# Performance work log

Hardware: AMD Instinct MI355X
Metric: run time of the kernel (lower is better)

Reference implementation:

```python
import jax, jax.numpy as jnp
import numpy as np

B, T, D, H = 4, 2048, 1024, 16
HD = D // H


def setup_inputs() -> dict:
    key = jax.random.key(0)
    k1, k2, k3 = jax.random.split(key, 3)
    x = jax.random.normal(k1, (B, T, D), dtype=jnp.float32)
    # xavier-uniform-like scale for the projections
    s_qkv = float(np.sqrt(6.0 / (D + 3 * D)))
    s_o = float(np.sqrt(6.0 / (D + D)))
    W_qkv = jax.random.uniform(k2, (D, 3 * D), minval=-s_qkv, maxval=s_qkv, dtype=jnp.float32)
    W_o = jax.random.uniform(k3, (D, D), minval=-s_o, maxval=s_o, dtype=jnp.float32)
    b_qkv = jnp.zeros((3 * D,), dtype=jnp.float32)
    b_o = jnp.zeros((D,), dtype=jnp.float32)
    # pad out the last 256 key positions to exercise the padding-mask path
    key_padding_mask = jnp.zeros((B, T), dtype=bool).at[:, -256:].set(True)
    return {"x": x, "W_qkv": W_qkv, "b_qkv": b_qkv, "W_o": W_o, "b_o": b_o,
            "key_padding_mask": key_padding_mask}


def reference(x, W_qkv, b_qkv, W_o, b_o, key_padding_mask):
    Bx, Tx, Dx = x.shape
    # fused QKV projection
    qkv = x @ W_qkv + b_qkv                      # [B,T,3D]
    q, k, v = jnp.split(qkv, 3, axis=-1)
    to_heads = lambda t: t.reshape(Bx, Tx, H, HD).transpose(0, 2, 1, 3)  # [B,H,T,Hd]
    q, k, v = to_heads(q), to_heads(k), to_heads(v)
    scale = 1.0 / np.sqrt(HD).astype(np.float32)
    scores = jnp.einsum('bhqd,bhkd->bhqk', q, k) * scale   # [B,H,T,T]
    causal = jnp.triu(jnp.ones((Tx, Tx), dtype=bool), k=1)  # True above diagonal => masked
    mask = key_padding_mask[:, None, None, :] | causal[None, None, :, :]
    scores = jnp.where(mask, -jnp.inf, scores)
    A = jax.nn.softmax(scores, axis=-1)
    ctx = jnp.einsum('bhqk,bhkd->bhqd', A, v)               # [B,H,T,Hd]
    y = ctx.transpose(0, 2, 1, 3).reshape(Bx, Tx, Dx)
    return y @ W_o + b_o
```

## Files before the change

kernel.cpp:

```cpp
#include <hip/hip_runtime.h>
#include <cstdint>
#include <cstddef>

typedef __bf16 bf16x8 __attribute__((ext_vector_type(8)));
typedef float f32x4 __attribute__((ext_vector_type(4)));
typedef float f32x16 __attribute__((ext_vector_type(16)));
typedef unsigned short u16x4 __attribute__((ext_vector_type(4)));
typedef unsigned int u32x4 __attribute__((ext_vector_type(4)));

__device__ __forceinline__ unsigned short f2bf(float f) {
  union { float f; unsigned u; } v; v.f = f;
  unsigned r = (v.u + 0x7FFF + ((v.u >> 16) & 1)) >> 16;
  return (unsigned short)r;
}

__device__ __forceinline__ unsigned pkbf(float x, float y) {
  unsigned short a = __builtin_bit_cast(unsigned short, (__bf16)x);
  unsigned short b = __builtin_bit_cast(unsigned short, (__bf16)y);
  return (unsigned)a | ((unsigned)b << 16);
}

__device__ __forceinline__ void gl2lds16(const void* g, void* l) {
  __builtin_amdgcn_global_load_lds(
      (const __attribute__((address_space(1))) void*)g,
      (__attribute__((address_space(3))) void*)l,
      16, 0, 0);
}

__global__ __launch_bounds__(256) void cast_f32_bf16(
    const float* __restrict__ in, unsigned short* __restrict__ out, int n) {
  int i = (blockIdx.x * 256 + threadIdx.x) * 4;
  if (i >= n) return;
  float4 v = *(const float4*)(in + i);
  u16x4 o;
  o[0] = f2bf(v.x); o[1] = f2bf(v.y); o[2] = f2bf(v.z); o[3] = f2bf(v.w);
  *(u16x4*)(out + i) = o;
}

__global__ __launch_bounds__(256) void transpose_cast(
    const float* __restrict__ in, unsigned short* __restrict__ out, int R, int C) {
  __shared__ float t[32][33];
  int c0 = blockIdx.x * 32, r0 = blockIdx.y * 32;
  int tx = threadIdx.x, ty = threadIdx.y;
#pragma unroll
  for (int j = 0; j < 4; ++j)
    t[ty + j * 8][tx] = in[(size_t)(r0 + ty + j * 8) * C + c0 + tx];
  __syncthreads();
#pragma unroll
  for (int j = 0; j < 4; ++j)
    out[(size_t)(c0 + ty + j * 8) * R + r0 + tx] = f2bf(t[tx][ty + j * 8]);
}

__global__ __launch_bounds__(256) void prep_pad(
    const int* __restrict__ mask, float* __restrict__ padd, int* __restrict__ kmax, int n) {
  int i = blockIdx.x * 256 + threadIdx.x;
  if (i >= n) return;
  int mv = mask[i];
  padd[i] = mv ? -1e30f : 0.0f;
  int key = mv ? 0 : ((i & 2047) + 1);
#pragma unroll
  for (int off = 32; off; off >>= 1) key = max(key, __shfl_xor(key, off, 64));
  if ((threadIdx.x & 63) == 0) atomicMax(&kmax[i >> 11], key);
}

template <int EPI>
__global__ __launch_bounds__(256) void gemm_bt(
    const unsigned short* __restrict__ A, const unsigned short* __restrict__ Bm,
    const float* __restrict__ bias, float* __restrict__ outF,
    unsigned short* __restrict__ Qb, unsigned short* __restrict__ Kb,
    unsigned short* __restrict__ Vt, int M, int N, int K) {
  __shared__ unsigned short As[2 * 128 * 32];
  __shared__ unsigned short Bs[2 * 128 * 32];
  const int tid = threadIdx.x;
  const int bm = blockIdx.x * 128;
  const int bn = blockIdx.y * 128;
  const int wave = tid >> 6, lane = tid & 63;
  const int wm = (wave >> 1) * 64, wn = (wave & 1) * 64;
  const int lr = lane & 15, lq = lane >> 4;

  f32x4 acc[4][4] = {};

  const int c0 = tid, c1 = tid + 256;
  const int rA0 = c0 >> 2, colA0 = (c0 & 3) * 8;
  const int rA1 = c1 >> 2, colA1 = (c1 & 3) * 8;

  auto stage = [&](int buf, int k0) {
    gl2lds16(A + (size_t)(bm + rA0) * K + k0 + colA0, As + buf * 4096 + c0 * 8);
    gl2lds16(A + (size_t)(bm + rA1) * K + k0 + colA1, As + buf * 4096 + c1 * 8);
    gl2lds16(Bm + (size_t)(bn + rA0) * K + k0 + colA0, Bs + buf * 4096 + c0 * 8);
    gl2lds16(Bm + (size_t)(bn + rA1) * K + k0 + colA1, Bs + buf * 4096 + c1 * 8);
  };

  stage(0, 0);
  int cur = 0;
  for (int k0 = 0; k0 < K; k0 += 32) {
    __syncthreads();
    if (k0 + 32 < K) stage(cur ^ 1, k0 + 32);
    const unsigned short* Asb = As + cur * 4096;
    const unsigned short* Bsb = Bs + cur * 4096;
    bf16x8 af[4], bfr[4];
#pragma unroll
    for (int mi = 0; mi < 4; ++mi)
      af[mi] = *(const bf16x8*)(Asb + (wm + mi * 16 + lr) * 32 + lq * 8);
#pragma unroll
    for (int nj = 0; nj < 4; ++nj)
      bfr[nj] = *(const bf16x8*)(Bsb + (wn + nj * 16 + lr) * 32 + lq * 8);
#pragma unroll
    for (int mi = 0; mi < 4; ++mi)
#pragma unroll
      for (int nj = 0; nj < 4; ++nj)
        acc[mi][nj] = __builtin_amdgcn_mfma_f32_16x16x32_bf16(af[mi], bfr[nj], acc[mi][nj], 0, 0, 0);
    cur ^= 1;
  }

#pragma unroll
  for (int mi = 0; mi < 4; ++mi) {
#pragma unroll
    for (int nj = 0; nj < 4; ++nj) {
#pragma unroll
      for (int r = 0; r < 4; ++r) {
        int m = bm + wm + mi * 16 + lq * 4 + r;
        int n = bn + wn + nj * 16 + lr;
        float v = acc[mi][nj][r] + bias[n];
        if (EPI == 0) {
          int b = m >> 11, t = m & 2047;
          int part = n >> 10, d = n & 1023;
          int h = d >> 6, hd = d & 63;
          size_t qk = ((size_t)(b * 16 + h) * 2048 + t) * 64 + hd;
          if (part == 0)      Qb[qk] = f2bf(v * 0.18033688011112042f);
          else if (part == 1) Kb[qk] = f2bf(v);
          else                Vt[((size_t)(b * 16 + h) * 64 + hd) * 2048 + t] = f2bf(v);
        } else {
          outF[(size_t)m * N + n] = v;
        }
      }
    }
  }
}

__global__ __launch_bounds__(256, 4) void flash_attn(
    const unsigned short* __restrict__ Qb, const unsigned short* __restrict__ Kb,
    const unsigned short* __restrict__ Vt, const int* __restrict__ kmax,
    unsigned short* __restrict__ ctx) {
  __shared__ unsigned short lds[16384];

  const int bid = blockIdx.x;
  const int halfg = bid >> 9;
  const int rb = bid & 511;
  const int bh = rb & 63;
  const int j0 = rb >> 6;
  const int j = halfg ? (15 - j0) : j0;
  const int blockQ = j << 7;
  const int b = bh >> 4, h = bh & 15;
  const int tid = threadIdx.x;
  const int wave = tid >> 6, lane = tid & 63;
  const int l31 = lane & 31, hi = lane >> 5;
  const int qw = blockQ + wave * 32;

  const unsigned short* Qh = Qb + (size_t)bh * 2048 * 64;
  const unsigned short* Kh = Kb + (size_t)bh * 2048 * 64;
  const unsigned short* Vh = Vt + (size_t)bh * 64 * 2048;
  unsigned short* ctxBase = ctx + (size_t)b * 2048 * 1024 + h * 64;

  const int kmaxRaw = kmax[b];
  const int kcapC = (kmaxRaw + 63) >> 6;
  const int lastB = min((blockQ + 127) >> 6, kcapC - 1);
  const int diagI = qw >> 6;

  bf16x8 qf[4];
#pragma unroll
  for (int ds = 0; ds < 4; ++ds)
    qf[ds] = *(const bf16x8*)(Qh + (size_t)(qw + l31) * 64 + ds * 16 + hi * 8);

  f32x16 O[2] = {};
  float mR = -1e30f, lR = 0.f;

  const int trow = tid >> 3, tslot = tid & 7;

  auto stage = [&](int bufI, int kcS) {
#pragma unroll
    for (int rnd = 0; rnd < 2; ++rnd) {
      int row = rnd * 32 + trow;
      int sl = tslot ^ (row & 7);
      gl2lds16(Kh + (size_t)(kcS + row) * 64 + sl * 8,
               lds + bufI * 8192 + rnd * 2048 + tid * 8);
      gl2lds16(Vh + (size_t)row * 2048 + kcS + sl * 8,
               lds + bufI * 8192 + 4096 + rnd * 2048 + tid * 8);
    }
  };

  stage(0, 0);
  int cur = 0;
  for (int i = 0; i <= lastB; ++i) {
    __syncthreads();
    if (i < lastB) stage(cur ^ 1, (i + 1) << 6);
    if (i <= diagI) {
      const int kc = i << 6;
      const unsigned short* Ksb = lds + cur * 8192;
      const unsigned short* Vsb = Ksb + 4096;

      f32x16 S[2] = {};
      __builtin_amdgcn_s_setprio(1);
#pragma unroll
      for (int kt = 0; kt < 2; ++kt) {
        const int row = kt * 32 + l31;
        const int rx = row & 7;
#pragma unroll
        for (int ds = 0; ds < 4; ++ds) {
          bf16x8 kfr = *(const bf16x8*)(Ksb + row * 64 + (((ds * 2 + hi) ^ rx) << 3));
          S[kt] = __builtin_amdgcn_mfma_f32_32x32x16_bf16(kfr, qf[ds], S[kt], 0, 0, 0);
        }
      }
      __builtin_amdgcn_s_setprio(0);

      const bool isDiag = (i == diagI);
      if (isDiag || (kc + 64 > kmaxRaw)) {
        const int q = qw + l31;
#pragma unroll
        for (int kt = 0; kt < 2; ++kt)
#pragma unroll
          for (int rr = 0; rr < 16; ++rr) {
            int key = kc + kt * 32 + (rr & 3) + ((rr >> 2) << 3) + (hi << 2);
            if ((isDiag && key > q) || key >= kmaxRaw) S[kt][rr] = -1e30f;
          }
      }

      {
        float v[16];
#pragma unroll
        for (int rr = 0; rr < 16; ++rr) v[rr] = fmaxf(S[0][rr], S[1][rr]);
#pragma unroll
        for (int st = 8; st; st >>= 1)
#pragma unroll
          for (int rr = 0; rr < st; ++rr) v[rr] = fmaxf(v[rr], v[rr + st]);
        float mx = fmaxf(v[0], __shfl_xor(v[0], 32, 64));
        float mnew = fmaxf(mR, mx);
        float a = __builtin_amdgcn_exp2f(mR - mnew);
        mR = mnew;
#pragma unroll
        for (int kt = 0; kt < 2; ++kt)
#pragma unroll
          for (int rr = 0; rr < 16; ++rr)
            S[kt][rr] = __builtin_amdgcn_exp2f(S[kt][rr] - mnew);
        float sacc[16];
#pragma unroll
        for (int rr = 0; rr < 16; ++rr) sacc[rr] = S[0][rr] + S[1][rr];
#pragma unroll
        for (int st = 8; st; st >>= 1)
#pragma unroll
          for (int rr = 0; rr < st; ++rr) sacc[rr] += sacc[rr + st];
        float sum = sacc[0] + __shfl_xor(sacc[0], 32, 64);
        lR = lR * a + sum;
#pragma unroll
        for (int mt = 0; mt < 2; ++mt)
#pragma unroll
          for (int rr = 0; rr < 16; ++rr) O[mt][rr] *= a;
      }
      bf16x8 pf[2][2];
#pragma unroll
      for (int kt = 0; kt < 2; ++kt) {
        unsigned a0 = pkbf(S[kt][0], S[kt][1]);
        unsigned a1 = pkbf(S[kt][2], S[kt][3]);
        unsigned b0 = pkbf(S[kt][4], S[kt][5]);
        unsigned b1 = pkbf(S[kt][6], S[kt][7]);
        unsigned c0 = pkbf(S[kt][8], S[kt][9]);
        unsigned c1 = pkbf(S[kt][10], S[kt][11]);
        unsigned d0 = pkbf(S[kt][12], S[kt][13]);
        unsigned d1 = pkbf(S[kt][14], S[kt][15]);
        unsigned s0 = __shfl_xor(hi ? a0 : b0, 32, 64);
        unsigned s1 = __shfl_xor(hi ? a1 : b1, 32, 64);
        unsigned s2 = __shfl_xor(hi ? c0 : d0, 32, 64);
        unsigned s3 = __shfl_xor(hi ? c1 : d1, 32, 64);
        u32x4 f0, f1;
        f0[0] = hi ? s0 : a0; f0[1] = hi ? s1 : a1;
        f0[2] = hi ? b0 : s0; f0[3] = hi ? b1 : s1;
        f1[0] = hi ? s2 : c0; f1[1] = hi ? s3 : c1;
        f1[2] = hi ? d0 : s2; f1[3] = hi ? d1 : s3;
        pf[kt][0] = __builtin_bit_cast(bf16x8, f0);
        pf[kt][1] = __builtin_bit_cast(bf16x8, f1);
      }

      __builtin_amdgcn_s_setprio(1);
      const int vx = l31 & 7;
#pragma unroll
      for (int kt = 0; kt < 2; ++kt)
#pragma unroll
        for (int ks = 0; ks < 2; ++ks) {
          const int slot = kt * 4 + ks * 2 + hi;
          bf16x8 v0 = *(const bf16x8*)(Vsb + l31 * 64 + ((slot ^ vx) << 3));
          bf16x8 v1 = *(const bf16x8*)(Vsb + (32 + l31) * 64 + ((slot ^ vx) << 3));
          O[0] = __builtin_amdgcn_mfma_f32_32x32x16_bf16(v0, pf[kt][ks], O[0], 0, 0, 0);
          O[1] = __builtin_amdgcn_mfma_f32_32x32x16_bf16(v1, pf[kt][ks], O[1], 0, 0, 0);
        }
      __builtin_amdgcn_s_setprio(0);
    }
    cur ^= 1;
  }

  {
    float linv = 1.0f / lR;
    const int q = qw + l31;
    unsigned short* cp = ctxBase + (size_t)q * 1024;
#pragma unroll
    for (int mt = 0; mt < 2; ++mt)
#pragma unroll
      for (int g = 0; g < 4; ++g) {
        u16x4 o4;
#pragma unroll
        for (int rr = 0; rr < 4; ++rr) o4[rr] = f2bf(O[mt][4 * g + rr] * linv);
        *(u16x4*)(cp + mt * 32 + 8 * g + 4 * hi) = o4;
      }
  }
}

extern "C" void kernel_launch(void* const* d_in, const int* in_sizes, int n_in,
                              void* d_out, int out_size, void* d_ws, size_t ws_size,
                              hipStream_t stream) {
  const float* x    = (const float*)d_in[0];
  const float* Wqkv = (const float*)d_in[1];
  const float* bqkv = (const float*)d_in[2];
  const float* Wo   = (const float*)d_in[3];
  const float* bo   = (const float*)d_in[4];
  const int*   mask = (const int*)d_in[5];
  float* out = (float*)d_out;

  unsigned short* ws = (unsigned short*)d_ws;
  const size_t SZ_X = (size_t)8192 * 1024;
  unsigned short* xb    = ws;
  unsigned short* WqkvT = xb + SZ_X;
  unsigned short* WoT   = WqkvT + (size_t)3072 * 1024;
  unsigned short* Qb    = WoT + (size_t)1024 * 1024;
  unsigned short* Kb    = Qb + SZ_X;
  unsigned short* Vt    = Kb + SZ_X;
  float*          padd  = (float*)(Vt + SZ_X);
  int*            kmax  = (int*)(padd + 8192);
  unsigned short* ctx   = xb;

  hipMemsetAsync(kmax, 0, 4 * sizeof(int), stream);
  cast_f32_bf16<<<8192, 256, 0, stream>>>(x, xb, (int)SZ_X);
  transpose_cast<<<dim3(96, 32), dim3(32, 8), 0, stream>>>(Wqkv, WqkvT, 1024, 3072);
  transpose_cast<<<dim3(32, 32), dim3(32, 8), 0, stream>>>(Wo, WoT, 1024, 1024);
  prep_pad<<<32, 256, 0, stream>>>(mask, padd, kmax, 8192);
  gemm_bt<0><<<dim3(64, 24), 256, 0, stream>>>(xb, WqkvT, bqkv, nullptr, Qb, Kb, Vt,
                                               8192, 3072, 1024);
  flash_attn<<<1024, 256, 0, stream>>>(Qb, Kb, Vt, kmax, ctx);
  gemm_bt<1><<<dim3(64, 8), 256, 0, stream>>>(ctx, WoT, bo, out, nullptr, nullptr, nullptr,
                                              8192, 1024, 1024);
}
```

Baseline: 273.7 us.

## Fuse preprocessing kernels and rework GEMM with triple-buffered swizzled LDS tiles

Merges the x cast, the two weight transpose-casts and the padding scan into one launch, and drops the unused padd buffer. The GEMM moves to 512-thread blocks with 256x128 tiles, a K-step of 64, and three LDS stages in dynamic shared memory. LDS rows use an XOR swizzle to avoid bank conflicts, and explicit vmcnt waits plus s_setprio around the MFMA burst help overlap loads with compute. This cuts launch overhead and raises GEMM data reuse and latency hiding, at the cost of large LDS use (144KB) that limits occupancy and fewer blocks for the output projection GEMM.

After: 261.6 us. 4.4% less time.

```diff
diff --git a/kernel.cpp b/kernel.cpp
--- a/kernel.cpp
+++ b/kernel.cpp
@@ -27,90 +27,128 @@
       16, 0, 0);
 }
 
-__global__ __launch_bounds__(256) void cast_f32_bf16(
-    const float* __restrict__ in, unsigned short* __restrict__ out, int n) {
-  int i = (blockIdx.x * 256 + threadIdx.x) * 4;
-  if (i >= n) return;
-  float4 v = *(const float4*)(in + i);
-  u16x4 o;
-  o[0] = f2bf(v.x); o[1] = f2bf(v.y); o[2] = f2bf(v.z); o[3] = f2bf(v.w);
-  *(u16x4*)(out + i) = o;
-}
-
-__global__ __launch_bounds__(256) void transpose_cast(
-    const float* __restrict__ in, unsigned short* __restrict__ out, int R, int C) {
+__global__ __launch_bounds__(256) void prep_fused(
+    const float* __restrict__ x, unsigned short* __restrict__ xb,
+    const float* __restrict__ Wqkv, unsigned short* __restrict__ WqkvT,
+    const float* __restrict__ Wo, unsigned short* __restrict__ WoT,
+    const int* __restrict__ mask, int* __restrict__ kmax) {
   __shared__ float t[32][33];
-  int c0 = blockIdx.x * 32, r0 = blockIdx.y * 32;
-  int tx = threadIdx.x, ty = threadIdx.y;
-#pragma unroll
-  for (int j = 0; j < 4; ++j)
-    t[ty + j * 8][tx] = in[(size_t)(r0 + ty + j * 8) * C + c0 + tx];
-  __syncthreads();
-#pragma unroll
-  for (int j = 0; j < 4; ++j)
-    out[(size_t)(c0 + ty + j * 8) * R + r0 + tx] = f2bf(t[tx][ty + j * 8]);
-}
-
-__global__ __launch_bounds__(256) void prep_pad(
-    const int* __restrict__ mask, float* __restrict__ padd, int* __restrict__ kmax, int n) {
-  int i = blockIdx.x * 256 + threadIdx.x;
-  if (i >= n) return;
-  int mv = mask[i];
-  padd[i] = mv ? -1e30f : 0.0f;
-  int key = mv ? 0 : ((i & 2047) + 1);
-#pragma unroll
-  for (int off = 32; off; off >>= 1) key = max(key, __shfl_xor(key, off, 64));
-  if ((threadIdx.x & 63) == 0) atomicMax(&kmax[i >> 11], key);
+  const int bid = blockIdx.x, tid = threadIdx.x;
+  if (bid < 4096) {
+    size_t i = ((size_t)bid * 256 + tid) * 4;
+#pragma unroll
+    for (int c = 0; c < 2; ++c) {
+      float4 v = *(const float4*)(x + i);
+      u16x4 o;
+      o[0] = f2bf(v.x); o[1] = f2bf(v.y); o[2] = f2bf(v.z); o[3] = f2bf(v.w);
+      *(u16x4*)(xb + i) = o;
+      i += (size_t)4096 * 256 * 4;
+    }
+  } else if (bid < 4096 + 3072) {
+    const int b2 = bid - 4096;
+    const int c0 = (b2 % 96) * 32, r0 = (b2 / 96) * 32;
+    const int tx = tid & 31, ty = tid >> 5;
+#pragma unroll
+    for (int j = 0; j < 4; ++j)
+      t[ty + j * 8][tx] = Wqkv[(size_t)(r0 + ty + j * 8) * 3072 + c0 + tx];
+    __syncthreads();
+#pragma unroll
+    for (int j = 0; j < 4; ++j)
+      WqkvT[(size_t)(c0 + ty + j * 8) * 1024 + r0 + tx] = f2bf(t[tx][ty + j * 8]);
+  } else if (bid < 8192) {
+    const int b3 = bid - (4096 + 3072);
+    const int c0 = (b3 & 31) * 32, r0 = (b3 >> 5) * 32;
+    const int tx = tid & 31, ty = tid >> 5;
+#pragma unroll
+    for (int j = 0; j < 4; ++j)
+      t[ty + j * 8][tx] = Wo[(size_t)(r0 + ty + j * 8) * 1024 + c0 + tx];
+    __syncthreads();
+#pragma unroll
+    for (int j = 0; j < 4; ++j)
+      WoT[(size_t)(c0 + ty + j * 8) * 1024 + r0 + tx] = f2bf(t[tx][ty + j * 8]);
+  } else {
+    const int i = (bid - 8192) * 256 + tid;
+    int mv = mask[i];
+    int key = mv ? 0 : ((i & 2047) + 1);
+#pragma unroll
+    for (int off = 32; off; off >>= 1) key = max(key, __shfl_xor(key, off, 64));
+    if ((tid & 63) == 0) atomicMax(&kmax[i >> 11], key);
+  }
 }
 
 template <int EPI>
-__global__ __launch_bounds__(256) void gemm_bt(
+__global__ __launch_bounds__(512, 2) void gemm_bt(
     const unsigned short* __restrict__ A, const unsigned short* __restrict__ Bm,
     const float* __restrict__ bias, float* __restrict__ outF,
     unsigned short* __restrict__ Qb, unsigned short* __restrict__ Kb,
     unsigned short* __restrict__ Vt, int M, int N, int K) {
-  __shared__ unsigned short As[2 * 128 * 32];
-  __shared__ unsigned short Bs[2 * 128 * 32];
+  extern __shared__ unsigned short lds[];
   const int tid = threadIdx.x;
-  const int bm = blockIdx.x * 128;
+  const int bm = blockIdx.x * 256;
   const int bn = blockIdx.y * 128;
   const int wave = tid >> 6, lane = tid & 63;
-  const int wm = (wave >> 1) * 64, wn = (wave & 1) * 64;
+  const int wm4 = wave >> 1, wn2 = wave & 1;
   const int lr = lane & 15, lq = lane >> 4;
+  const int NT = K >> 6;
 
   f32x4 acc[4][4] = {};
 
-  const int c0 = tid, c1 = tid + 256;
-  const int rA0 = c0 >> 2, colA0 = (c0 & 3) * 8;
-  const int rA1 = c1 >> 2, colA1 = (c1 & 3) * 8;
+  const int tr = tid >> 3, ts = tid & 7;
+  const int srcsl = (ts ^ (tr & 7)) << 3;
 
   auto stage = [&](int buf, int k0) {
-    gl2lds16(A + (size_t)(bm + rA0) * K + k0 + colA0, As + buf * 4096 + c0 * 8);
-    gl2lds16(A + (size_t)(bm + rA1) * K + k0 + colA1, As + buf * 4096 + c1 * 8);
-    gl2lds16(Bm + (size_t)(bn + rA0) * K + k0 + colA0, Bs + buf * 4096 + c0 * 8);
-    gl2lds16(Bm + (size_t)(bn + rA1) * K + k0 + colA1, Bs + buf * 4096 + c1 * 8);
+#pragma unroll
+    for (int r = 0; r < 4; ++r) {
+      int row = r * 64 + tr;
+      gl2lds16(A + (size_t)(bm + row) * K + k0 + srcsl,
+               lds + buf * 24576 + r * 4096 + tid * 8);
+    }
+#pragma unroll
+    for (int r = 0; r < 2; ++r) {
+      int row = r * 64 + tr;
+      gl2lds16(Bm + (size_t)(bn + row) * K + k0 + srcsl,
+               lds + buf * 24576 + 16384 + r * 4096 + tid * 8);
+    }
   };
 
   stage(0, 0);
-  int cur = 0;
-  for (int k0 = 0; k0 < K; k0 += 32) {
-    __syncthreads();
-    if (k0 + 32 < K) stage(cur ^ 1, k0 + 32);
-    const unsigned short* Asb = As + cur * 4096;
-    const unsigned short* Bsb = Bs + cur * 4096;
-    bf16x8 af[4], bfr[4];
-#pragma unroll
-    for (int mi = 0; mi < 4; ++mi)
-      af[mi] = *(const bf16x8*)(Asb + (wm + mi * 16 + lr) * 32 + lq * 8);
-#pragma unroll
-    for (int nj = 0; nj < 4; ++nj)
-      bfr[nj] = *(const bf16x8*)(Bsb + (wn + nj * 16 + lr) * 32 + lq * 8);
-#pragma unroll
-    for (int mi = 0; mi < 4; ++mi)
-#pragma unroll
-      for (int nj = 0; nj < 4; ++nj)
-        acc[mi][nj] = __builtin_amdgcn_mfma_f32_16x16x32_bf16(af[mi], bfr[nj], acc[mi][nj], 0, 0, 0);
-    cur ^= 1;
+  stage(1, 64);
+  int bT = 0, bT2 = 2;
+  const int rx = lr & 7;
+  for (int T = 0; T < NT; ++T) {
+    if (T < NT - 1) {
+      asm volatile("s_waitcnt vmcnt(6)" ::: "memory");
+    } else {
+      asm volatile("s_waitcnt vmcnt(0)" ::: "memory");
+    }
+    __builtin_amdgcn_s_barrier();
+    __builtin_amdgcn_sched_barrier(0);
+    if (T + 2 < NT) stage(bT2, (T + 2) << 6);
+    const unsigned short* Ab = lds + bT * 24576;
+    const unsigned short* Bb = Ab + 16384;
+#pragma unroll
+    for (int ks = 0; ks < 2; ++ks) {
+      bf16x8 afr[4], bfr[4];
+#pragma unroll
+      for (int mi = 0; mi < 4; ++mi) {
+        int row = wm4 * 64 + mi * 16 + lr;
+        afr[mi] = *(const bf16x8*)(Ab + row * 64 + ((((ks << 2) | lq) ^ rx) << 3));
+      }
+#pragma unroll
+      for (int nj = 0; nj < 4; ++nj) {
+        int row = wn2 * 64 + nj * 16 + lr;
+        bfr[nj] = *(const bf16x8*)(Bb + row * 64 + ((((ks << 2) | lq) ^ rx) << 3));
+      }
+      __builtin_amdgcn_s_setprio(1);
+#pragma unroll
+      for (int mi = 0; mi < 4; ++mi)
+#pragma unroll
+        for (int nj = 0; nj < 4; ++nj)
+          acc[mi][nj] = __builtin_amdgcn_mfma_f32_16x16x32_bf16(afr[mi], bfr[nj], acc[mi][nj], 0, 0, 0);
+      __builtin_amdgcn_s_setprio(0);
+    }
+    bT = (bT == 2) ? 0 : bT + 1;
+    bT2 = (bT2 == 2) ? 0 : bT2 + 1;
   }
 
 #pragma unroll
@@ -119,8 +157,8 @@
     for (int nj = 0; nj < 4; ++nj) {
 #pragma unroll
       for (int r = 0; r < 4; ++r) {
-        int m = bm + wm + mi * 16 + lq * 4 + r;
-        int n = bn + wn + nj * 16 + lr;
+        int m = bm + wm4 * 64 + mi * 16 + lq * 4 + r;
+        int n = bn + wn2 * 64 + nj * 16 + lr;
         float v = acc[mi][nj][r] + bias[n];
         if (EPI == 0) {
           int b = m >> 11, t = m & 2047;
@@ -332,18 +370,23 @@
   unsigned short* Qb    = WoT + (size_t)1024 * 1024;
   unsigned short* Kb    = Qb + SZ_X;
   unsigned short* Vt    = Kb + SZ_X;
-  float*          padd  = (float*)(Vt + SZ_X);
-  int*            kmax  = (int*)(padd + 8192);
+  int*            kmax  = (int*)(Vt + SZ_X);
   unsigned short* ctx   = xb;
 
+  static bool inited = false;
+  if (!inited) {
+    hipFuncSetAttribute((const void*)gemm_bt<0>,
+                        hipFuncAttributeMaxDynamicSharedMemorySize, 147456);
+    hipFuncSetAttribute((const void*)gemm_bt<1>,
+                        hipFuncAttributeMaxDynamicSharedMemorySize, 147456);
+    inited = true;
+  }
+
   hipMemsetAsync(kmax, 0, 4 * sizeof(int), stream);
-  cast_f32_bf16<<<8192, 256, 0, stream>>>(x, xb, (int)SZ_X);
-  transpose_cast<<<dim3(96, 32), dim3(32, 8), 0, stream>>>(Wqkv, WqkvT, 1024, 3072);
-  transpose_cast<<<dim3(32, 32), dim3(32, 8), 0, stream>>>(Wo, WoT, 1024, 1024);
-  prep_pad<<<32, 256, 0, stream>>>(mask, padd, kmax, 8192);
-  gemm_bt<0><<<dim3(64, 24), 256, 0, stream>>>(xb, WqkvT, bqkv, nullptr, Qb, Kb, Vt,
-                                               8192, 3072, 1024);
+  prep_fused<<<8224, 256, 0, stream>>>(x, xb, Wqkv, WqkvT, Wo, WoT, mask, kmax);
+  gemm_bt<0><<<dim3(32, 24), 512, 147456, stream>>>(xb, WqkvT, bqkv, nullptr, Qb, Kb, Vt,
+                                                    8192, 3072, 1024);
   flash_attn<<<1024, 256, 0, stream>>>(Qb, Kb, Vt, kmax, ctx);
-  gemm_bt<1><<<dim3(64, 8), 256, 0, stream>>>(ctx, WoT, bo, out, nullptr, nullptr, nullptr,
-                                              8192, 1024, 1024);
-}
+  gemm_bt<1><<<dim3(32, 8), 512, 147456, stream>>>(ctx, WoT, bo, out, nullptr, nullptr, nullptr,
+                                                   8192, 1024, 1024);
+}
```
